# Kernel tuning notes

Measured on AMD Instinct MI355X. Metric: run time of the kernel, lower is better.

The kernel has to match this reference:

```python
import jax, jax.numpy as jnp
import numpy as np

N = 50000
E = 500000
IN_DIM = 384
HID = 256
HEADS = 4
OUT_DIM = 128
NEG_SLOPE = 0.2


def _glorot(key, shape):
    fan_in, fan_out = shape[0], shape[-1]
    lim = jnp.sqrt(6.0 / (fan_in + fan_out))
    return jax.random.uniform(key, shape, jnp.float32, -lim, lim)


def setup_inputs() -> dict:
    key = jax.random.key(0)
    ks = jax.random.split(key, 16)
    x = jax.random.normal(ks[0], (N, IN_DIM), jnp.float32)
    node_attr = jax.random.normal(ks[1], (N, 2), jnp.float32)
    edge_index = jax.random.randint(ks[2], (2, E), 0, N, jnp.int64)
    return {
        "x": x,
        "node_attr": node_attr,
        "edge_index": edge_index,
        # node_encoder: Linear(386 -> 384)
        "enc_W": _glorot(ks[3], (IN_DIM + 2, IN_DIM)),
        "enc_b": jnp.zeros((IN_DIM,), jnp.float32),
        # gat1: 384 -> 4 heads x 256, concat
        "W1": _glorot(ks[4], (IN_DIM, HEADS * HID)),
        "a_src1": _glorot(ks[5], (HEADS, HID)),
        "a_dst1": _glorot(ks[6], (HEADS, HID)),
        "b1": jnp.zeros((HEADS * HID,), jnp.float32),
        # gat2: 1024 -> 1 head x 128, mean (concat=False)
        "W2": _glorot(ks[7], (HEADS * HID, OUT_DIM)),
        "a_src2": _glorot(ks[8], (1, OUT_DIM)),
        "a_dst2": _glorot(ks[9], (1, OUT_DIM)),
        "b2": jnp.zeros((OUT_DIM,), jnp.float32),
    }


def gat_conv(x, src, dst, W, a_src, a_dst, bias, heads, out_ch, concat):
    # x: [N, F]; src/dst: [E'] (self-loops already included)
    n = x.shape[0]
    h = (x @ W).reshape(n, heads, out_ch)          # [N, H, C]
    alpha_s = jnp.einsum('nhc,hc->nh', h, a_src)   # [N, H]
    alpha_d = jnp.einsum('nhc,hc->nh', h, a_dst)
    e = alpha_s[src] + alpha_d[dst]                # [E', H]
    e = jnp.where(e >= 0, e, NEG_SLOPE * e)        # LeakyReLU(0.2)
    # segment softmax over incoming edges of each destination node
    m = jax.ops.segment_max(e, dst, num_segments=n)
    e = jnp.exp(e - m[dst])
    denom = jax.ops.segment_sum(e, dst, num_segments=n)
    alpha = e / (denom[dst] + 1e-16)               # [E', H]
    msg = h[src] * alpha[:, :, None]               # [E', H, C]
    out = jax.ops.segment_sum(msg, dst, num_segments=n)  # [N, H, C]
    out = out.reshape(n, heads * out_ch) if concat else out.mean(axis=1)
    return out + bias


def reference(x, node_attr, edge_index, enc_W, enc_b,
              W1, a_src1, a_dst1, b1, W2, a_src2, a_dst2, b2):
    n = x.shape[0]
    # node encoder on [x ; node_attr]
    h = jnp.concatenate([x, node_attr], axis=-1) @ enc_W + enc_b
    # add self-loops once (PyG GATConv default add_self_loops=True)
    loop = jnp.arange(n, dtype=edge_index.dtype)
    src = jnp.concatenate([edge_index[0], loop])
    dst = jnp.concatenate([edge_index[1], loop])
    h = gat_conv(h, src, dst, W1, a_src1, a_dst1, b1, HEADS, HID, True)
    h = jax.nn.elu(h)
    out = gat_conv(h, src, dst, W2, a_src2, a_dst2, b2, 1, OUT_DIM, False)
    return out
```

## Files before the change

kernel.cpp:

```cpp
#include <hip/hip_runtime.h>
#include <hip/hip_bf16.h>
#include <type_traits>


#define NN 50000
#define NE 500000
#define EP (NE + NN)

typedef __hip_bfloat16 bf16;
typedef short short8 __attribute__((ext_vector_type(8)));
typedef __bf16 bf16x8 __attribute__((ext_vector_type(8)));
typedef float f32x4 __attribute__((ext_vector_type(4)));

__device__ __forceinline__ float b2f(bf16 v) { return __bfloat162float(v); }
__device__ __forceinline__ bf16  f2b(float v) { return __float2bfloat16(v); }
__device__ __forceinline__ unsigned short f2bu(float v) {
  bf16 b = __float2bfloat16(v);
  return *reinterpret_cast<unsigned short*>(&b);
}

__device__ __forceinline__ float ldf(const void* p, size_t i, bool f32) {
  return f32 ? ((const float*)p)[i] : b2f(((const bf16*)p)[i]);
}

__device__ __forceinline__ float bflo(unsigned u) { return __uint_as_float(u << 16); }
__device__ __forceinline__ float bfhi(unsigned u) { return __uint_as_float(u & 0xffff0000u); }

__device__ __forceinline__ float leaky(float v) { return v >= 0.f ? v : 0.2f * v; }

__global__ void k_detect_edge(const unsigned int* __restrict__ w, unsigned int* __restrict__ flag) {
  unsigned int acc = 0;
  for (int i = blockIdx.x * 256 + threadIdx.x; i < NE; i += gridDim.x * 256)
    acc |= w[2 * i + 1];
  if (acc) atomicOr(flag, 1u);
}

__global__ void k_detect_f32(const unsigned int* __restrict__ w, unsigned int* __restrict__ flag) {
  unsigned int acc = 0;
  for (int i = blockIdx.x * 256 + threadIdx.x; i < (1 << 20); i += gridDim.x * 256) {
    unsigned int e = (w[i] >> 7) & 0xFF;
    if (e > 0xA0) acc = 1;
  }
  if (acc) atomicOr(flag, 1u);
}

__global__ void k_convert(const int* __restrict__ ei, const unsigned int* __restrict__ flag,
                          int* __restrict__ esrc, int* __restrict__ edst,
                          int* __restrict__ deg) {
  int e = blockIdx.x * 256 + threadIdx.x;
  if (e >= EP) return;
  int s, d;
  if (e < NE) {
    if (*flag) { s = ei[e]; d = ei[NE + e]; }
    else { const long long* e64 = (const long long*)ei; s = (int)e64[e]; d = (int)e64[NE + e]; }
    s = min(max(s, 0), NN - 1);
    d = min(max(d, 0), NN - 1);
  } else {
    s = d = e - NE;
  }
  esrc[e] = s;
  edst[e] = d;
  atomicAdd(&deg[d], 1);
}

__global__ void k_pack_cat(const void* __restrict__ x, const void* __restrict__ na,
                           bf16* __restrict__ catp, const unsigned int* __restrict__ fflag) {
  const bool f32 = (*fflag != 0);
  const int total = NN * 104;
  for (int g = blockIdx.x * 256 + threadIdx.x; g < total; g += gridDim.x * 256) {
    int n = g / 104, r = g - n * 104;
    int c = r * 4;
    float v0 = 0.f, v1 = 0.f, v2 = 0.f, v3 = 0.f;
    if (c < 384) {
      if (f32) {
        const float4 f = *(const float4*)((const float*)x + (size_t)n * 384 + c);
        v0 = f.x; v1 = f.y; v2 = f.z; v3 = f.w;
      } else {
        const bf16* xb = (const bf16*)x + (size_t)n * 384 + c;
        v0 = b2f(xb[0]); v1 = b2f(xb[1]); v2 = b2f(xb[2]); v3 = b2f(xb[3]);
      }
    } else if (c == 384) {
      v0 = ldf(na, (size_t)n * 2 + 0, f32);
      v1 = ldf(na, (size_t)n * 2 + 1, f32);
    }
    ushort2 o0, o1;
    o0.x = f2bu(v0); o0.y = f2bu(v1);
    o1.x = f2bu(v2); o1.y = f2bu(v3);
    ushort2* dst = (ushort2*)((unsigned short*)catp + (size_t)n * 416 + c);
    dst[0] = o0; dst[1] = o1;
  }
}

__global__ void k_pack_w(const void* __restrict__ W, bf16* __restrict__ Wp,
                         int K, int Kpad, int N, const unsigned int* __restrict__ fflag) {
  const bool f32 = (*fflag != 0);
  int total = Kpad * N;
  for (int i = blockIdx.x * 256 + threadIdx.x; i < total; i += gridDim.x * 256) {
    int kb = i / (N * 32);
    int rem = i - kb * N * 32;
    int n = rem >> 5, kk = rem & 31;
    int k = kb * 32 + kk;
    float v = (k < K) ? ldf(W, (size_t)k * N + n, f32) : 0.f;
    Wp[i] = f2b(v);
  }
}

template<bool ADD_BIAS, bool ALPHA, int NH, typename CT>
__global__ __launch_bounds__(256) void gemm_mfma(
    const bf16* __restrict__ A, int lda,
    const bf16* __restrict__ Bp,
    const void* __restrict__ bias,
    const void* __restrict__ a_srcp, const void* __restrict__ a_dstp,
    float* __restrict__ as_out, float* __restrict__ ad_out,
    CT* __restrict__ C,
    int M, int N, int K,
    const unsigned int* __restrict__ fflag) {
  const bool xf32 = (ADD_BIAS || ALPHA) ? (*fflag != 0) : false;
  __shared__ short As[128 * 40];
  __shared__ short Bs[128 * 40];
  const int t = threadIdx.x;
  const int lane = t & 63, wave = t >> 6;
  const int wm = wave & 1, wn = wave >> 1;
  const int quad = lane >> 4, l15 = lane & 15;
  const int m0 = blockIdx.x * 128, n0 = blockIdx.y * 128;

  f32x4 acc[4][4];
#pragma unroll
  for (int i = 0; i < 4; ++i)
#pragma unroll
    for (int j = 0; j < 4; ++j) acc[i][j] = (f32x4){0.f, 0.f, 0.f, 0.f};

  for (int k0 = 0; k0 < K; k0 += 32) {
#pragma unroll
    for (int i = 0; i < 2; ++i) {
      int c = t + i * 256;
      int row = c >> 2, koff = (c & 3) * 8;
      int gm = min(m0 + row, M - 1);
      const short* src = (const short*)A + (size_t)gm * lda + k0 + koff;
      *(short8*)&As[row * 40 + koff] = *(const short8*)src;
    }
    {
      const short* base = (const short*)Bp + ((size_t)(k0 >> 5) * N + n0) * 32;
#pragma unroll
      for (int i = 0; i < 2; ++i) {
        int c = t + i * 256;
        int nl = c >> 2, koff = (c & 3) * 8;
        *(short8*)&Bs[nl * 40 + koff] = *(const short8*)(base + nl * 32 + koff);
      }
    }
    __syncthreads();
    bf16x8 af[4], bfr[4];
#pragma unroll
    for (int mi = 0; mi < 4; ++mi)
      af[mi] = *reinterpret_cast<const bf16x8*>(&As[(wm * 64 + mi * 16 + l15) * 40 + quad * 8]);
#pragma unroll
    for (int ni = 0; ni < 4; ++ni)
      bfr[ni] = *reinterpret_cast<const bf16x8*>(&Bs[(wn * 64 + ni * 16 + l15) * 40 + quad * 8]);
#pragma unroll
    for (int mi = 0; mi < 4; ++mi)
#pragma unroll
      for (int ni = 0; ni < 4; ++ni)
        acc[mi][ni] = __builtin_amdgcn_mfma_f32_16x16x32_bf16(af[mi], bfr[ni], acc[mi][ni], 0, 0, 0);
    __syncthreads();
  }

#pragma unroll
  for (int mi = 0; mi < 4; ++mi) {
#pragma unroll
    for (int ni = 0; ni < 4; ++ni) {
      const int gn = n0 + wn * 64 + ni * 16 + l15;
      float bv = ADD_BIAS ? ldf(bias, gn, xf32) : 0.f;
#pragma unroll
      for (int r = 0; r < 4; ++r) {
        const int gm = m0 + wm * 64 + mi * 16 + quad * 4 + r;
        if (gm < M) {
          float v = acc[mi][ni][r] + bv;
          if constexpr (std::is_same<CT, float>::value)
            C[(size_t)gm * N + gn] = v;
          else
            C[(size_t)gm * N + gn] = f2b(v);
        }
      }
    }
  }

  if (ALPHA) {
    float avs[4], avd[4];
#pragma unroll
    for (int ni = 0; ni < 4; ++ni) {
      const int gn = n0 + wn * 64 + ni * 16 + l15;
      avs[ni] = ldf(a_srcp, gn, xf32);
      avd[ni] = ldf(a_dstp, gn, xf32);
    }
    const int head = (n0 + wn * 64) >> 8;
#pragma unroll
    for (int mi = 0; mi < 4; ++mi) {
#pragma unroll
      for (int r = 0; r < 4; ++r) {
        float ps = 0.f, pd = 0.f;
#pragma unroll
        for (int ni = 0; ni < 4; ++ni) {
          const float v = acc[mi][ni][r];
          ps = fmaf(v, avs[ni], ps);
          pd = fmaf(v, avd[ni], pd);
        }
#pragma unroll
        for (int off = 8; off > 0; off >>= 1) {
          ps += __shfl_down(ps, off, 16);
          pd += __shfl_down(pd, off, 16);
        }
        if (l15 == 0) {
          const int gm = m0 + wm * 64 + mi * 16 + quad * 4 + r;
          if (gm < M) {
            atomicAdd(&as_out[gm * NH + head], ps);
            atomicAdd(&ad_out[gm * NH + head], pd);
          }
        }
      }
    }
  }
}

#define SCAN_B 512
#define SCAN_NB ((NN + SCAN_B - 1) / SCAN_B)

__global__ __launch_bounds__(SCAN_B) void k_scan1(const int* __restrict__ deg,
                                                  int* __restrict__ row_ptr,
                                                  int* __restrict__ partial) {
  int b = blockIdx.x, t = threadIdx.x;
  int i = b * SCAN_B + t;
  int v = (i < NN) ? deg[i] : 0;
  int lane = t & 63, w = t >> 6;
  int x = v;
#pragma unroll
  for (int off = 1; off < 64; off <<= 1) {
    int y = __shfl_up(x, off, 64);
    if (lane >= off) x += y;
  }
  __shared__ int ws[8];
  if (lane == 63) ws[w] = x;
  __syncthreads();
  if (t == 0) {
    int run = 0;
#pragma unroll
    for (int j = 0; j < 8; ++j) { int tmp = ws[j]; ws[j] = run; run += tmp; }
    partial[b] = run;
  }
  __syncthreads();
  int excl = x - v + ws[w];
  if (i < NN) row_ptr[i] = excl;
}

__global__ void k_scan2(int* __restrict__ partial, int* __restrict__ row_ptr) {
  if (blockIdx.x == 0 && threadIdx.x == 0) {
    int run = 0;
    for (int j = 0; j < SCAN_NB; ++j) { int tmp = partial[j]; partial[j] = run; run += tmp; }
    row_ptr[NN] = run;
  }
}

__global__ __launch_bounds__(SCAN_B) void k_scan3(const int* __restrict__ partial,
                                                  int* __restrict__ row_ptr,
                                                  int* __restrict__ cursor) {
  int b = blockIdx.x, t = threadIdx.x;
  int i = b * SCAN_B + t;
  if (i < NN) {
    int v = row_ptr[i] + partial[b];
    row_ptr[i] = v;
    cursor[i] = v;
  }
}

__global__ void k_scatter(const int* __restrict__ esrc, const int* __restrict__ edst,
                          int* __restrict__ cursor, int* __restrict__ csr) {
  int e = blockIdx.x * 256 + threadIdx.x;
  if (e >= EP) return;
  int pos = atomicAdd(&cursor[edst[e]], 1);
  pos = min(max(pos, 0), EP - 1);
  csr[pos] = esrc[e];
}

__global__ __launch_bounds__(256) void k_agg1(
    const int* __restrict__ csr, const int* __restrict__ row_ptr,
    const float* __restrict__ as1, const float* __restrict__ ad1,
    const bf16* __restrict__ h1, const void* __restrict__ b1,
    bf16* __restrict__ act1, const unsigned int* __restrict__ fflag) {
  const bool f32 = (*fflag != 0);
  const int n = blockIdx.x, t = threadIdx.x;
  const int w = t >> 6, l = t & 63;
  const int start = row_ptr[n], end = row_ptr[n + 1];
  const float adn = ad1[n * 4 + w];
  const unsigned* hb = (const unsigned*)h1;
  const int coff = w * 128 + l * 2;

  float a0 = 0.f, a1 = 0.f, a2 = 0.f, a3 = 0.f, densum = 0.f;

  int idx = start;
  for (; idx + 4 <= end; idx += 4) {
    int s0 = csr[idx], s1 = csr[idx + 1], s2 = csr[idx + 2], s3 = csr[idx + 3];
    uint2 w0 = *(const uint2*)(hb + (size_t)s0 * 512 + coff);
    uint2 w1 = *(const uint2*)(hb + (size_t)s1 * 512 + coff);
    uint2 w2 = *(const uint2*)(hb + (size_t)s2 * 512 + coff);
    uint2 w3 = *(const uint2*)(hb + (size_t)s3 * 512 + coff);
    float p0 = __expf(leaky(as1[s0 * 4 + w] + adn));
    float p1 = __expf(leaky(as1[s1 * 4 + w] + adn));
    float p2 = __expf(leaky(as1[s2 * 4 + w] + adn));
    float p3 = __expf(leaky(as1[s3 * 4 + w] + adn));
    densum += (p0 + p1) + (p2 + p3);
    a0 = fmaf(bflo(w0.x), p0, a0); a1 = fmaf(bfhi(w0.x), p0, a1);
    a2 = fmaf(bflo(w0.y), p0, a2); a3 = fmaf(bfhi(w0.y), p0, a3);
    a0 = fmaf(bflo(w1.x), p1, a0); a1 = fmaf(bfhi(w1.x), p1, a1);
    a2 = fmaf(bflo(w1.y), p1, a2); a3 = fmaf(bfhi(w1.y), p1, a3);
    a0 = fmaf(bflo(w2.x), p2, a0); a1 = fmaf(bfhi(w2.x), p2, a1);
    a2 = fmaf(bflo(w2.y), p2, a2); a3 = fmaf(bfhi(w2.y), p2, a3);
    a0 = fmaf(bflo(w3.x), p3, a0); a1 = fmaf(bfhi(w3.x), p3, a1);
    a2 = fmaf(bflo(w3.y), p3, a2); a3 = fmaf(bfhi(w3.y), p3, a3);
  }
  for (; idx < end; ++idx) {
    int s0 = csr[idx];
    uint2 w0 = *(const uint2*)(hb + (size_t)s0 * 512 + coff);
    float p0 = __expf(leaky(as1[s0 * 4 + w] + adn));
    densum += p0;
    a0 = fmaf(bflo(w0.x), p0, a0); a1 = fmaf(bfhi(w0.x), p0, a1);
    a2 = fmaf(bflo(w0.y), p0, a2); a3 = fmaf(bfhi(w0.y), p0, a3);
  }

  const float inv = 1.f / (densum + 1e-16f);
  const int col = w * 256 + l * 4;
  float v0 = a0 * inv + ldf(b1, col + 0, f32);
  float v1 = a1 * inv + ldf(b1, col + 1, f32);
  float v2 = a2 * inv + ldf(b1, col + 2, f32);
  float v3 = a3 * inv + ldf(b1, col + 3, f32);
  v0 = v0 > 0.f ? v0 : expm1f(v0);
  v1 = v1 > 0.f ? v1 : expm1f(v1);
  v2 = v2 > 0.f ? v2 : expm1f(v2);
  v3 = v3 > 0.f ? v3 : expm1f(v3);
  ushort2 o0, o1;
  o0.x = f2bu(v0); o0.y = f2bu(v1);
  o1.x = f2bu(v2); o1.y = f2bu(v3);
  ushort2* orow = (ushort2*)((unsigned short*)act1 + (size_t)n * 1024 + col);
  orow[0] = o0; orow[1] = o1;
}

__global__ __launch_bounds__(256) void k_agg2(
    const int* __restrict__ csr, const int* __restrict__ row_ptr,
    const float* __restrict__ as2, const float* __restrict__ ad2,
    const bf16* __restrict__ h2, const void* __restrict__ b2v,
    float* __restrict__ out, const unsigned int* __restrict__ fflag) {
  const bool f32 = (*fflag != 0);
  const int n = blockIdx.x, t = threadIdx.x;
  const int g = t >> 5, tc = t & 31;
  const int start = row_ptr[n], end = row_ptr[n + 1];
  const float adn = ad2[n];
  const unsigned* hb = (const unsigned*)h2;
  float a0 = 0.f, a1 = 0.f, a2 = 0.f, a3 = 0.f, densum = 0.f;

  for (int idx = start + g; idx < end; idx += 8) {
    int s = csr[idx];
    const uint2 w = *(const uint2*)(hb + (size_t)s * 64 + tc * 2);
    float pe = __expf(leaky(as2[s] + adn));
    densum += pe;
    a0 = fmaf(bflo(w.x), pe, a0); a1 = fmaf(bfhi(w.x), pe, a1);
    a2 = fmaf(bflo(w.y), pe, a2); a3 = fmaf(bfhi(w.y), pe, a3);
  }

  __shared__ float4 red[8][32];
  __shared__ float dsum[8];
  if (g > 0) {
    red[g][tc] = make_float4(a0, a1, a2, a3);
    if (tc == 0) dsum[g] = densum;
  }
  __syncthreads();
  if (g == 0) {
#pragma unroll
    for (int j = 1; j < 8; ++j) {
      const float4 o = red[j][tc];
      a0 += o.x; a1 += o.y; a2 += o.z; a3 += o.w;
      densum += dsum[j];
    }
    const float inv = 1.f / (densum + 1e-16f);
    float* orow = out + (size_t)n * 128 + tc * 4;
    orow[0] = a0 * inv + ldf(b2v, tc * 4 + 0, f32);
    orow[1] = a1 * inv + ldf(b2v, tc * 4 + 1, f32);
    orow[2] = a2 * inv + ldf(b2v, tc * 4 + 2, f32);
    orow[3] = a3 * inv + ldf(b2v, tc * 4 + 3, f32);
  }
}

extern "C" void kernel_launch(void* const* d_in, const int* in_sizes, int n_in,
                              void* d_out, int out_size, void* d_ws, size_t ws_size,
                              hipStream_t stream) {
  const void* x       = d_in[0];
  const void* na      = d_in[1];
  const int*  ei      = (const int*)d_in[2];
  const void* enc_W   = d_in[3];
  const void* enc_b   = d_in[4];
  const void* W1      = d_in[5];
  const void* a_src1  = d_in[6];
  const void* a_dst1  = d_in[7];
  const void* b1      = d_in[8];
  const void* W2      = d_in[9];
  const void* a_src2  = d_in[10];
  const void* a_dst2  = d_in[11];
  const void* b2      = d_in[12];
  float* out = (float*)d_out;

  size_t off = 0;
  char* ws = (char*)d_ws;
  auto alloc = [&](size_t bytes) -> void* {
    void* p = ws + off;
    off += (bytes + 255) & ~(size_t)255;
    return p;
  };
  bf16*  h1      = (bf16*)alloc((size_t)NN * 1024 * 2);
  bf16*  act1    = (bf16*)alloc((size_t)NN * 1024 * 2);
  bf16*  catp    = act1;
  bf16*  h0      = (bf16*)alloc((size_t)NN * 384 * 2);
  bf16*  h2      = (bf16*)alloc((size_t)NN * 128 * 2);
  bf16*  encWp   = (bf16*)alloc((size_t)416 * 384 * 2);
  bf16*  W1p     = (bf16*)alloc((size_t)384 * 1024 * 2);
  bf16*  W2p     = (bf16*)alloc((size_t)1024 * 128 * 2);
  int*   esrc    = (int*)alloc((size_t)EP * 4);
  int*   edst    = (int*)alloc((size_t)EP * 4);
  unsigned int* eflag = (unsigned int*)alloc(4);
  unsigned int* fflag = (unsigned int*)alloc(4);
  int*   csr     = (int*)alloc((size_t)EP * 4);
  float* as1     = (float*)alloc((size_t)NN * 4 * 4);
  float* ad1     = (float*)alloc((size_t)NN * 4 * 4);
  float* as2     = (float*)alloc((size_t)NN * 4);
  float* ad2     = (float*)alloc((size_t)NN * 4);
  int*   deg     = (int*)alloc((size_t)NN * 4);
  int*   row_ptr = (int*)alloc((size_t)(NN + 1) * 4);
  int*   cursor  = (int*)alloc((size_t)NN * 4);
  int*   partial = (int*)alloc((size_t)SCAN_NB * 4);
  (void)ws_size; (void)in_sizes; (void)n_in; (void)out_size;

  (void)hipMemsetAsync(eflag, 0, 4,               stream);
  (void)hipMemsetAsync(fflag, 0, 4,               stream);
  (void)hipMemsetAsync(deg,   0, (size_t)NN * 4,  stream);
  (void)hipMemsetAsync(as1,   0, (size_t)NN * 16, stream);
  (void)hipMemsetAsync(ad1,   0, (size_t)NN * 16, stream);
  (void)hipMemsetAsync(as2,   0, (size_t)NN * 4,  stream);
  (void)hipMemsetAsync(ad2,   0, (size_t)NN * 4,  stream);

  const int EB = (EP + 255) / 256;
  const int MB = (NN + 127) / 128;

  k_detect_edge<<<512, 256, 0, stream>>>((const unsigned int*)ei, eflag);
  k_detect_f32<<<512, 256, 0, stream>>>((const unsigned int*)x, fflag);

  k_convert<<<EB, 256, 0, stream>>>(ei, eflag, esrc, edst, deg);
  k_scan1<<<SCAN_NB, SCAN_B, 0, stream>>>(deg, row_ptr, partial);
  k_scan2<<<1, 64, 0, stream>>>(partial, row_ptr);
  k_scan3<<<SCAN_NB, SCAN_B, 0, stream>>>(partial, row_ptr, cursor);
  k_scatter<<<EB, 256, 0, stream>>>(esrc, edst, cursor, csr);

  k_pack_cat<<<8192, 256, 0, stream>>>(x, na, catp, fflag);
  k_pack_w<<<1024, 256, 0, stream>>>(enc_W, encWp, 386, 416, 384, fflag);
  k_pack_w<<<1024, 256, 0, stream>>>(W1, W1p, 384, 384, 1024, fflag);
  k_pack_w<<<1024, 256, 0, stream>>>(W2, W2p, 1024, 1024, 128, fflag);

  gemm_mfma<true, false, 1, bf16><<<dim3(MB, 3), 256, 0, stream>>>(
      catp, 416, encWp, enc_b, nullptr, nullptr, nullptr, nullptr,
      h0, NN, 384, 416, fflag);
  gemm_mfma<false, true, 4, bf16><<<dim3(MB, 8), 256, 0, stream>>>(
      h0, 384, W1p, nullptr, a_src1, a_dst1, as1, ad1,
      h1, NN, 1024, 384, fflag);

  k_agg1<<<NN, 256, 0, stream>>>(csr, row_ptr, as1, ad1, h1, b1, act1, fflag);

  gemm_mfma<false, true, 1, bf16><<<dim3(MB, 1), 256, 0, stream>>>(
      act1, 1024, W2p, nullptr, a_src2, a_dst2, as2, ad2,
      h2, NN, 128, 1024, fflag);

  k_agg2<<<NN, 256, 0, stream>>>(csr, row_ptr, as2, ad2, h2, b2, out, fflag);
}
```

Before: 704.4 us.

## Map one wavefront per destination node in GAT aggregation kernels

Both aggregation kernels now assign one 64-lane wavefront per destination node, with four nodes per block, instead of a whole 256-thread block per node. The edge index is made wave-uniform via readfirstlane, and each lane loads 16 bf16 features with two 16-byte loads. agg2 drops its shared-memory reduction and barrier. Fewer blocks and wider loads aim to cut launch and scheduling overhead and improve gather efficiency, though each wave now walks its whole edge list serially with more registers per lane.

After: 702.9 us. About the same (-0.2%).

```diff
diff --git a/kernel.cpp b/kernel.cpp
--- a/kernel.cpp
+++ b/kernel.cpp
@@ -27,6 +27,17 @@
 __device__ __forceinline__ float bfhi(unsigned u) { return __uint_as_float(u & 0xffff0000u); }
 
 __device__ __forceinline__ float leaky(float v) { return v >= 0.f ? v : 0.2f * v; }
+
+__device__ __forceinline__ void acc8(float* acc, uint4 w, float p) {
+  acc[0] = fmaf(bflo(w.x), p, acc[0]);
+  acc[1] = fmaf(bfhi(w.x), p, acc[1]);
+  acc[2] = fmaf(bflo(w.y), p, acc[2]);
+  acc[3] = fmaf(bfhi(w.y), p, acc[3]);
+  acc[4] = fmaf(bflo(w.z), p, acc[4]);
+  acc[5] = fmaf(bfhi(w.z), p, acc[5]);
+  acc[6] = fmaf(bflo(w.w), p, acc[6]);
+  acc[7] = fmaf(bfhi(w.w), p, acc[7]);
+}
 
 __global__ void k_detect_edge(const unsigned int* __restrict__ w, unsigned int* __restrict__ flag) {
   unsigned int acc = 0;
@@ -286,60 +297,56 @@
     const bf16* __restrict__ h1, const void* __restrict__ b1,
     bf16* __restrict__ act1, const unsigned int* __restrict__ fflag) {
   const bool f32 = (*fflag != 0);
-  const int n = blockIdx.x, t = threadIdx.x;
-  const int w = t >> 6, l = t & 63;
+  const int t = threadIdx.x;
+  const int wv = t >> 6, l = t & 63;
+  const int n = blockIdx.x * 4 + wv;
+  const int h = l >> 4;
   const int start = row_ptr[n], end = row_ptr[n + 1];
-  const float adn = ad1[n * 4 + w];
+  const float adn = ad1[n * 4 + h];
   const unsigned* hb = (const unsigned*)h1;
-  const int coff = w * 128 + l * 2;
-
-  float a0 = 0.f, a1 = 0.f, a2 = 0.f, a3 = 0.f, densum = 0.f;
+
+  float acc[16];
+#pragma unroll
+  for (int j = 0; j < 16; ++j) acc[j] = 0.f;
+  float densum = 0.f;
 
   int idx = start;
-  for (; idx + 4 <= end; idx += 4) {
-    int s0 = csr[idx], s1 = csr[idx + 1], s2 = csr[idx + 2], s3 = csr[idx + 3];
-    uint2 w0 = *(const uint2*)(hb + (size_t)s0 * 512 + coff);
-    uint2 w1 = *(const uint2*)(hb + (size_t)s1 * 512 + coff);
-    uint2 w2 = *(const uint2*)(hb + (size_t)s2 * 512 + coff);
-    uint2 w3 = *(const uint2*)(hb + (size_t)s3 * 512 + coff);
-    float p0 = __expf(leaky(as1[s0 * 4 + w] + adn));
-    float p1 = __expf(leaky(as1[s1 * 4 + w] + adn));
-    float p2 = __expf(leaky(as1[s2 * 4 + w] + adn));
-    float p3 = __expf(leaky(as1[s3 * 4 + w] + adn));
-    densum += (p0 + p1) + (p2 + p3);
-    a0 = fmaf(bflo(w0.x), p0, a0); a1 = fmaf(bfhi(w0.x), p0, a1);
-    a2 = fmaf(bflo(w0.y), p0, a2); a3 = fmaf(bfhi(w0.y), p0, a3);
-    a0 = fmaf(bflo(w1.x), p1, a0); a1 = fmaf(bfhi(w1.x), p1, a1);
-    a2 = fmaf(bflo(w1.y), p1, a2); a3 = fmaf(bfhi(w1.y), p1, a3);
-    a0 = fmaf(bflo(w2.x), p2, a0); a1 = fmaf(bfhi(w2.x), p2, a1);
-    a2 = fmaf(bflo(w2.y), p2, a2); a3 = fmaf(bfhi(w2.y), p2, a3);
-    a0 = fmaf(bflo(w3.x), p3, a0); a1 = fmaf(bfhi(w3.x), p3, a1);
-    a2 = fmaf(bflo(w3.y), p3, a2); a3 = fmaf(bfhi(w3.y), p3, a3);
-  }
-  for (; idx < end; ++idx) {
-    int s0 = csr[idx];
-    uint2 w0 = *(const uint2*)(hb + (size_t)s0 * 512 + coff);
-    float p0 = __expf(leaky(as1[s0 * 4 + w] + adn));
+  for (; idx + 2 <= end; idx += 2) {
+    const int s0 = __builtin_amdgcn_readfirstlane(csr[idx]);
+    const int s1 = __builtin_amdgcn_readfirstlane(csr[idx + 1]);
+    const uint4* r0 = (const uint4*)(hb + (size_t)s0 * 512);
+    const uint4* r1 = (const uint4*)(hb + (size_t)s1 * 512);
+    const uint4 a0 = r0[2 * l], c0 = r0[2 * l + 1];
+    const uint4 a1 = r1[2 * l], c1 = r1[2 * l + 1];
+    const float p0 = __expf(leaky(as1[s0 * 4 + h] + adn));
+    const float p1 = __expf(leaky(as1[s1 * 4 + h] + adn));
+    densum += p0 + p1;
+    acc8(acc, a0, p0); acc8(acc + 8, c0, p0);
+    acc8(acc, a1, p1); acc8(acc + 8, c1, p1);
+  }
+  if (idx < end) {
+    const int s0 = __builtin_amdgcn_readfirstlane(csr[idx]);
+    const uint4* r0 = (const uint4*)(hb + (size_t)s0 * 512);
+    const uint4 a0 = r0[2 * l], c0 = r0[2 * l + 1];
+    const float p0 = __expf(leaky(as1[s0 * 4 + h] + adn));
     densum += p0;
-    a0 = fmaf(bflo(w0.x), p0, a0); a1 = fmaf(bfhi(w0.x), p0, a1);
-    a2 = fmaf(bflo(w0.y), p0, a2); a3 = fmaf(bfhi(w0.y), p0, a3);
+    acc8(acc, a0, p0); acc8(acc + 8, c0, p0);
   }
 
   const float inv = 1.f / (densum + 1e-16f);
-  const int col = w * 256 + l * 4;
-  float v0 = a0 * inv + ldf(b1, col + 0, f32);
-  float v1 = a1 * inv + ldf(b1, col + 1, f32);
-  float v2 = a2 * inv + ldf(b1, col + 2, f32);
-  float v3 = a3 * inv + ldf(b1, col + 3, f32);
-  v0 = v0 > 0.f ? v0 : expm1f(v0);
-  v1 = v1 > 0.f ? v1 : expm1f(v1);
-  v2 = v2 > 0.f ? v2 : expm1f(v2);
-  v3 = v3 > 0.f ? v3 : expm1f(v3);
-  ushort2 o0, o1;
-  o0.x = f2bu(v0); o0.y = f2bu(v1);
-  o1.x = f2bu(v2); o1.y = f2bu(v3);
-  ushort2* orow = (ushort2*)((unsigned short*)act1 + (size_t)n * 1024 + col);
-  orow[0] = o0; orow[1] = o1;
+  const int col = l * 16;
+  unsigned ow[8];
+#pragma unroll
+  for (int j = 0; j < 8; ++j) {
+    float v0 = acc[2 * j]     * inv + ldf(b1, col + 2 * j,     f32);
+    float v1 = acc[2 * j + 1] * inv + ldf(b1, col + 2 * j + 1, f32);
+    v0 = v0 > 0.f ? v0 : expm1f(v0);
+    v1 = v1 > 0.f ? v1 : expm1f(v1);
+    ow[j] = (unsigned)f2bu(v0) | ((unsigned)f2bu(v1) << 16);
+  }
+  uint4* orow = (uint4*)((unsigned short*)act1 + (size_t)n * 1024 + col);
+  orow[0] = *(uint4*)&ow[0];
+  orow[1] = *(uint4*)&ow[4];
 }
 
 __global__ __launch_bounds__(256) void k_agg2(
@@ -348,43 +355,39 @@
     const bf16* __restrict__ h2, const void* __restrict__ b2v,
     float* __restrict__ out, const unsigned int* __restrict__ fflag) {
   const bool f32 = (*fflag != 0);
-  const int n = blockIdx.x, t = threadIdx.x;
-  const int g = t >> 5, tc = t & 31;
+  const int t = threadIdx.x;
+  const int wv = t >> 6, l = t & 63;
+  const int n = blockIdx.x * 4 + wv;
   const int start = row_ptr[n], end = row_ptr[n + 1];
   const float adn = ad2[n];
   const unsigned* hb = (const unsigned*)h2;
-  float a0 = 0.f, a1 = 0.f, a2 = 0.f, a3 = 0.f, densum = 0.f;
-
-  for (int idx = start + g; idx < end; idx += 8) {
-    int s = csr[idx];
-    const uint2 w = *(const uint2*)(hb + (size_t)s * 64 + tc * 2);
-    float pe = __expf(leaky(as2[s] + adn));
-    densum += pe;
-    a0 = fmaf(bflo(w.x), pe, a0); a1 = fmaf(bfhi(w.x), pe, a1);
-    a2 = fmaf(bflo(w.y), pe, a2); a3 = fmaf(bfhi(w.y), pe, a3);
-  }
-
-  __shared__ float4 red[8][32];
-  __shared__ float dsum[8];
-  if (g > 0) {
-    red[g][tc] = make_float4(a0, a1, a2, a3);
-    if (tc == 0) dsum[g] = densum;
-  }
-  __syncthreads();
-  if (g == 0) {
-#pragma unroll
-    for (int j = 1; j < 8; ++j) {
-      const float4 o = red[j][tc];
-      a0 += o.x; a1 += o.y; a2 += o.z; a3 += o.w;
-      densum += dsum[j];
-    }
-    const float inv = 1.f / (densum + 1e-16f);
-    float* orow = out + (size_t)n * 128 + tc * 4;
-    orow[0] = a0 * inv + ldf(b2v, tc * 4 + 0, f32);
-    orow[1] = a1 * inv + ldf(b2v, tc * 4 + 1, f32);
-    orow[2] = a2 * inv + ldf(b2v, tc * 4 + 2, f32);
-    orow[3] = a3 * inv + ldf(b2v, tc * 4 + 3, f32);
-  }
+  float a0 = 0.f, a1 = 0.f, densum = 0.f;
+
+  int idx = start;
+  for (; idx + 2 <= end; idx += 2) {
+    const int s0 = __builtin_amdgcn_readfirstlane(csr[idx]);
+    const int s1 = __builtin_amdgcn_readfirstlane(csr[idx + 1]);
+    const unsigned w0 = hb[(size_t)s0 * 64 + l];
+    const unsigned w1 = hb[(size_t)s1 * 64 + l];
+    const float p0 = __expf(leaky(as2[s0] + adn));
+    const float p1 = __expf(leaky(as2[s1] + adn));
+    densum += p0 + p1;
+    a0 = fmaf(bflo(w0), p0, a0); a1 = fmaf(bfhi(w0), p0, a1);
+    a0 = fmaf(bflo(w1), p1, a0); a1 = fmaf(bfhi(w1), p1, a1);
+  }
+  if (idx < end) {
+    const int s0 = __builtin_amdgcn_readfirstlane(csr[idx]);
+    const unsigned w0 = hb[(size_t)s0 * 64 + l];
+    const float p0 = __expf(leaky(as2[s0] + adn));
+    densum += p0;
+    a0 = fmaf(bflo(w0), p0, a0); a1 = fmaf(bfhi(w0), p0, a1);
+  }
+
+  const float inv = 1.f / (densum + 1e-16f);
+  float2 o;
+  o.x = a0 * inv + ldf(b2v, l * 2 + 0, f32);
+  o.y = a1 * inv + ldf(b2v, l * 2 + 1, f32);
+  *(float2*)(out + (size_t)n * 128 + l * 2) = o;
 }
 
 extern "C" void kernel_launch(void* const* d_in, const int* in_sizes, int n_in,
@@ -467,11 +470,11 @@
       h0, 384, W1p, nullptr, a_src1, a_dst1, as1, ad1,
       h1, NN, 1024, 384, fflag);
 
-  k_agg1<<<NN, 256, 0, stream>>>(csr, row_ptr, as1, ad1, h1, b1, act1, fflag);
+  k_agg1<<<NN / 4, 256, 0, stream>>>(csr, row_ptr, as1, ad1, h1, b1, act1, fflag);
 
   gemm_mfma<false, true, 1, bf16><<<dim3(MB, 1), 256, 0, stream>>>(
       act1, 1024, W2p, nullptr, a_src2, a_dst2, as2, ad2,
       h2, NN, 128, 1024, fflag);
 
-  k_agg2<<<NN, 256, 0, stream>>>(csr, row_ptr, as2, ad2, h2, b2, out, fflag);
-}
+  k_agg2<<<NN / 4, 256, 0, stream>>>(csr, row_ptr, as2, ad2, h2, b2, out, fflag);
+}
```

## Use one wavefront per node in layer-2 aggregation and nontemporal stores

Applied to the files above, without the earlier changes.

The layer-2 aggregation kernel now maps one 64-lane wavefront per destination node, with four nodes per block. Each lane owns two output channels. The edge loop is unrolled by two with wave-uniform source indices, which removes the shared-memory cross-group reduction and the __syncthreads. Both aggregation kernels now write their outputs with 64-bit nontemporal stores. The trade-off is less parallelism per node for high-degree nodes, in exchange for fewer blocks and no block-level sync.

After: 695.2 us. Within noise of the previous version (-1.3%).

```diff
diff --git a/kernel.cpp b/kernel.cpp
--- a/kernel.cpp
+++ b/kernel.cpp
@@ -335,11 +335,11 @@
   v1 = v1 > 0.f ? v1 : expm1f(v1);
   v2 = v2 > 0.f ? v2 : expm1f(v2);
   v3 = v3 > 0.f ? v3 : expm1f(v3);
-  ushort2 o0, o1;
-  o0.x = f2bu(v0); o0.y = f2bu(v1);
-  o1.x = f2bu(v2); o1.y = f2bu(v3);
-  ushort2* orow = (ushort2*)((unsigned short*)act1 + (size_t)n * 1024 + col);
-  orow[0] = o0; orow[1] = o1;
+  unsigned lo = (unsigned)f2bu(v0) | ((unsigned)f2bu(v1) << 16);
+  unsigned hi = (unsigned)f2bu(v2) | ((unsigned)f2bu(v3) << 16);
+  unsigned long long ow = (unsigned long long)lo | ((unsigned long long)hi << 32);
+  __builtin_nontemporal_store(
+      ow, (unsigned long long*)((unsigned short*)act1 + (size_t)n * 1024 + col));
 }
 
 __global__ __launch_bounds__(256) void k_agg2(
@@ -348,43 +348,41 @@
     const bf16* __restrict__ h2, const void* __restrict__ b2v,
     float* __restrict__ out, const unsigned int* __restrict__ fflag) {
   const bool f32 = (*fflag != 0);
-  const int n = blockIdx.x, t = threadIdx.x;
-  const int g = t >> 5, tc = t & 31;
+  const int t = threadIdx.x;
+  const int wv = t >> 6, l = t & 63;
+  const int n = blockIdx.x * 4 + wv;
   const int start = row_ptr[n], end = row_ptr[n + 1];
   const float adn = ad2[n];
   const unsigned* hb = (const unsigned*)h2;
-  float a0 = 0.f, a1 = 0.f, a2 = 0.f, a3 = 0.f, densum = 0.f;
-
-  for (int idx = start + g; idx < end; idx += 8) {
-    int s = csr[idx];
-    const uint2 w = *(const uint2*)(hb + (size_t)s * 64 + tc * 2);
-    float pe = __expf(leaky(as2[s] + adn));
-    densum += pe;
-    a0 = fmaf(bflo(w.x), pe, a0); a1 = fmaf(bfhi(w.x), pe, a1);
-    a2 = fmaf(bflo(w.y), pe, a2); a3 = fmaf(bfhi(w.y), pe, a3);
-  }
-
-  __shared__ float4 red[8][32];
-  __shared__ float dsum[8];
-  if (g > 0) {
-    red[g][tc] = make_float4(a0, a1, a2, a3);
-    if (tc == 0) dsum[g] = densum;
-  }
-  __syncthreads();
-  if (g == 0) {
-#pragma unroll
-    for (int j = 1; j < 8; ++j) {
-      const float4 o = red[j][tc];
-      a0 += o.x; a1 += o.y; a2 += o.z; a3 += o.w;
-      densum += dsum[j];
-    }
-    const float inv = 1.f / (densum + 1e-16f);
-    float* orow = out + (size_t)n * 128 + tc * 4;
-    orow[0] = a0 * inv + ldf(b2v, tc * 4 + 0, f32);
-    orow[1] = a1 * inv + ldf(b2v, tc * 4 + 1, f32);
-    orow[2] = a2 * inv + ldf(b2v, tc * 4 + 2, f32);
-    orow[3] = a3 * inv + ldf(b2v, tc * 4 + 3, f32);
-  }
+  float a0 = 0.f, a1 = 0.f, densum = 0.f;
+
+  int idx = start;
+  for (; idx + 2 <= end; idx += 2) {
+    const int s0 = __builtin_amdgcn_readfirstlane(csr[idx]);
+    const int s1 = __builtin_amdgcn_readfirstlane(csr[idx + 1]);
+    const unsigned w0 = hb[(size_t)s0 * 64 + l];
+    const unsigned w1 = hb[(size_t)s1 * 64 + l];
+    const float p0 = __expf(leaky(as2[s0] + adn));
+    const float p1 = __expf(leaky(as2[s1] + adn));
+    densum += p0 + p1;
+    a0 = fmaf(bflo(w0), p0, a0); a1 = fmaf(bfhi(w0), p0, a1);
+    a0 = fmaf(bflo(w1), p1, a0); a1 = fmaf(bfhi(w1), p1, a1);
+  }
+  if (idx < end) {
+    const int s0 = __builtin_amdgcn_readfirstlane(csr[idx]);
+    const unsigned w0 = hb[(size_t)s0 * 64 + l];
+    const float p0 = __expf(leaky(as2[s0] + adn));
+    densum += p0;
+    a0 = fmaf(bflo(w0), p0, a0); a1 = fmaf(bfhi(w0), p0, a1);
+  }
+
+  const float inv = 1.f / (densum + 1e-16f);
+  float2 o;
+  o.x = a0 * inv + ldf(b2v, l * 2 + 0, f32);
+  o.y = a1 * inv + ldf(b2v, l * 2 + 1, f32);
+  unsigned long long u;
+  __builtin_memcpy(&u, &o, 8);
+  __builtin_nontemporal_store(u, (unsigned long long*)(out + (size_t)n * 128 + l * 2));
 }
 
 extern "C" void kernel_launch(void* const* d_in, const int* in_sizes, int n_in,
@@ -473,5 +471,5 @@
       act1, 1024, W2p, nullptr, a_src2, a_dst2, as2, ad2,
       h2, NN, 128, 1024, fflag);
 
-  k_agg2<<<NN, 256, 0, stream>>>(csr, row_ptr, as2, ad2, h2, b2, out, fflag);
-}
+  k_agg2<<<NN / 4, 256, 0, stream>>>(csr, row_ptr, as2, ad2, h2, b2, out, fflag);
+}
```
